# Kernel optimization log

Measured on AMD Instinct MI355X. Metric: run time of the kernel, lower is better.

Reference implementation:

```python
import jax, jax.numpy as jnp
import numpy as np

B, N, C, H, W = 4, 8, 48, 128, 128
DIM = N * C  # 384, must equal in_dim


def conv1x1(x, w, b):
    # x: (B, Cin, H, W), w: (Cout, Cin, 1, 1)
    y = jax.lax.conv_general_dilated(
        x, w, window_strides=(1, 1), padding='VALID',
        dimension_numbers=('NCHW', 'OIHW', 'NCHW'))
    return y + b[None, :, None, None]


def dwconv3x3(x, w, b):
    # depthwise: w: (Cg, 1, 3, 3), groups = Cg
    y = jax.lax.conv_general_dilated(
        x, w, window_strides=(1, 1), padding=((1, 1), (1, 1)),
        dimension_numbers=('NCHW', 'OIHW', 'NCHW'),
        feature_group_count=w.shape[0])
    return y + b[None, :, None, None]


def setup_inputs() -> dict:
    key = jax.random.key(0)
    ks = jax.random.split(key, 4)
    s = 0.02
    return {
        'x': jax.random.normal(ks[0], (B, N, C, H, W), jnp.float32),
        'temperature': jnp.ones((1,), jnp.float32),
        'w_qkv': jax.random.normal(ks[1], (3 * DIM, DIM, 1, 1), jnp.float32) * s,
        'b_qkv': jnp.zeros((3 * DIM,), jnp.float32),
        'w_dw': jax.random.normal(ks[2], (3 * DIM, 1, 3, 3), jnp.float32) * s,
        'b_dw': jnp.zeros((3 * DIM,), jnp.float32),
        'w_proj': jax.random.normal(ks[3], (DIM, DIM, 1, 1), jnp.float32) * s,
        'b_proj': jnp.zeros((DIM,), jnp.float32),
    }


def reference(x, temperature, w_qkv, b_qkv, w_dw, b_dw, w_proj, b_proj):
    b, n, c, h, w = x.shape
    x_in = x.reshape(b, n * c, h, w)
    qkv = dwconv3x3(conv1x1(x_in, w_qkv, b_qkv), w_dw, b_dw)  # (b, 3*n*c, h, w)
    q, k, v = jnp.split(qkv, 3, axis=1)

    def flat(t):
        return t.reshape(b, n, -1)  # (b, n, c*h*w)

    def l2n(t):
        # torch F.normalize: x / max(||x||_2, eps)
        nrm = jnp.sqrt(jnp.sum(t * t, axis=-1, keepdims=True))
        return t / jnp.maximum(nrm, 1e-12)

    q = l2n(flat(q))
    k = l2n(flat(k))
    v = flat(v)
    attn = jax.nn.softmax(jnp.einsum('bnd,bmd->bnm', q, k) * temperature, axis=-1)  # (b, n, n)
    out = jnp.einsum('bnm,bmd->bnd', attn, v).reshape(b, n * c, h, w)
    out = conv1x1(out, w_proj, b_proj)
    out = out.reshape(b, n, c, h, w) + x  # residual
    return out.reshape(b, n * c, h, w)
```

## Files before the change

kernel.cpp:

```cpp
#include <hip/hip_runtime.h>
#include <hip/hip_bf16.h>

#define BB 4
#define CPG 48
#define HH 128
#define WW2 128
#define PP 16384
#define DIM 384
#define DIM3 1152

typedef unsigned short u16;
typedef __attribute__((ext_vector_type(8))) short bf16x8;
typedef __attribute__((ext_vector_type(4))) float f32x4;

__device__ __forceinline__ float bf2f(u16 u) {
    return __uint_as_float(((unsigned int)u) << 16);
}
__device__ __forceinline__ u16 f2bf(float f) {
    unsigned int u = __float_as_uint(f);
    unsigned int r = (u + 0x7fffu + ((u >> 16) & 1u)) >> 16;
    return (u16)r;
}

__device__ __forceinline__ int swz(int row, int kb) {
    return row * 128 + (kb ^ ((row & 7) << 4));
}

__device__ __forceinline__ void gld_lds16(const u16* g, char* l) {
    __builtin_amdgcn_global_load_lds(
        (const __attribute__((address_space(1))) void*)g,
        (__attribute__((address_space(3))) void*)l, 16, 0, 0);
}

__global__ __launch_bounds__(256) void k_wcvt(const float* __restrict__ w,
                                              u16* __restrict__ wbf)
{
    const int i4 = (blockIdx.x * 256 + threadIdx.x) * 4;
    float4 v = *reinterpret_cast<const float4*>(w + i4);
    ushort4 s;
    s.x = f2bf(v.x); s.y = f2bf(v.y); s.z = f2bf(v.z); s.w = f2bf(v.w);
    *reinterpret_cast<ushort4*>(wbf + i4) = s;
}

__global__ __launch_bounds__(256) void k_tr_x(const float* __restrict__ x,
                                              u16* __restrict__ xt)
{
    const int b = blockIdx.z;
    const int k0 = blockIdx.y * 64;
    const int p0 = blockIdx.x * 64;
    const int t = threadIdx.x;
    __shared__ u16 T[64][68];

    const int kl = t >> 4;
    const int pl = (t & 15) * 4;
#pragma unroll
    for (int ks = 0; ks < 4; ++ks) {
        const int k = ks * 16 + kl;
        float4 v = *reinterpret_cast<const float4*>(&x[((size_t)b * DIM + k0 + k) * PP + p0 + pl]);
        ushort4 s;
        s.x = f2bf(v.x); s.y = f2bf(v.y); s.z = f2bf(v.z); s.w = f2bf(v.w);
        *reinterpret_cast<ushort4*>(&T[k][pl]) = s;
    }
    __syncthreads();
    const int pr = t >> 2;
    const int kg = (t & 3) * 16;
    __align__(16) u16 tmp[16];
#pragma unroll
    for (int j = 0; j < 16; ++j) tmp[j] = T[kg + j][pr];
    u16* dst = xt + ((size_t)b * PP + p0 + pr) * DIM + k0 + kg;
    *reinterpret_cast<uint4*>(dst)     = *reinterpret_cast<uint4*>(tmp);
    *reinterpret_cast<uint4*>(dst + 8) = *reinterpret_cast<uint4*>(tmp + 8);
}

template<int MODE>
__global__ __launch_bounds__(256) void k_gemm(const u16* __restrict__ A, int aStride,
                                              const u16* __restrict__ Bt,
                                              const float* __restrict__ bias,
                                              u16* __restrict__ ybf,
                                              const float* __restrict__ xres,
                                              float* __restrict__ fout,
                                              int nyTiles)
{
    const int bid = blockIdx.x;
    const int xcd = bid & 7;
    const int r1  = bid >> 3;
    const int px  = xcd * 16 + (r1 & 15);
    const int r2  = r1 >> 4;
    const int b   = r2 / nyTiles;
    const int yt  = r2 - b * nyTiles;
    const int co0 = yt * 128;
    const int p0  = px * 128;

    const int t   = threadIdx.x;
    const int l   = t & 63;
    const int wid = t >> 6;
    const int wr  = wid >> 1;
    const int wc  = wid & 1;
    const int lr  = l & 15;
    const int lg  = l >> 4;

    __shared__ __align__(16) char lds[32768];
    char* AsB = lds;
    char* BsB = lds + 16384;

    f32x4 acc[4][4];
#pragma unroll
    for (int m = 0; m < 4; ++m)
#pragma unroll
        for (int n = 0; n < 4; ++n) acc[m][n] = (f32x4){0.f, 0.f, 0.f, 0.f};

    const u16* Ab  = A  + (size_t)b * aStride;
    const u16* Btb = Bt + (size_t)b * PP * DIM;

    const int lrow8 = l >> 3;
    const int sl    = l & 7;

    for (int k0 = 0; k0 < DIM; k0 += 64) {
        if (k0) __syncthreads();
#pragma unroll
        for (int i = 0; i < 4; ++i) {
            const int rbase = wid * 32 + i * 8;
            const int row   = rbase + lrow8;
            const int elem  = (sl * 8) ^ ((row & 7) << 3);
            gld_lds16(Ab  + (size_t)(co0 + row) * DIM + k0 + elem, AsB + rbase * 128);
            gld_lds16(Btb + (size_t)(p0  + row) * DIM + k0 + elem, BsB + rbase * 128);
        }
        __syncthreads();

#pragma unroll
        for (int kk = 0; kk < 64; kk += 32) {
            const int kbyte = kk * 2 + lg * 16;
            bf16x8 av[4], bv[4];
#pragma unroll
            for (int m = 0; m < 4; ++m) {
                const int row = wr * 64 + m * 16 + lr;
                av[m] = *reinterpret_cast<const bf16x8*>(AsB + swz(row, kbyte));
            }
#pragma unroll
            for (int n = 0; n < 4; ++n) {
                const int row = wc * 64 + n * 16 + lr;
                bv[n] = *reinterpret_cast<const bf16x8*>(BsB + swz(row, kbyte));
            }
#pragma unroll
            for (int m = 0; m < 4; ++m)
#pragma unroll
                for (int n = 0; n < 4; ++n)
                    acc[m][n] = __builtin_amdgcn_mfma_f32_16x16x32_bf16(
                        av[m], bv[n], acc[m][n], 0, 0, 0);
        }
    }

    float bias_r[4][4];
#pragma unroll
    for (int m = 0; m < 4; ++m)
#pragma unroll
        for (int r = 0; r < 4; ++r)
            bias_r[m][r] = bias[co0 + wr * 64 + m * 16 + lg * 4 + r];

    if (MODE == 0) {
        __syncthreads();
        u16* Cs = reinterpret_cast<u16*>(lds);
#pragma unroll
        for (int m = 0; m < 4; ++m)
#pragma unroll
            for (int n = 0; n < 4; ++n)
#pragma unroll
                for (int r = 0; r < 4; ++r) {
                    const int row = wr * 64 + m * 16 + lg * 4 + r;
                    const int col = wc * 64 + n * 16 + lr;
                    Cs[row * 128 + col] = f2bf(acc[m][n][r] + bias_r[m][r]);
                }
        __syncthreads();
        const int rr = t >> 4;
        const int cs = (t & 15) * 8;
#pragma unroll
        for (int j = 0; j < 8; ++j) {
            const int row = j * 16 + rr;
            *reinterpret_cast<uint4*>(&ybf[((size_t)b * DIM3 + co0 + row) * PP + p0 + cs]) =
                *reinterpret_cast<const uint4*>(&Cs[row * 128 + cs]);
        }
    } else {
        float* Cf = reinterpret_cast<float*>(lds);
#pragma unroll
        for (int h = 0; h < 2; ++h) {
            __syncthreads();
            if (wr == h) {
#pragma unroll
                for (int m = 0; m < 4; ++m)
#pragma unroll
                    for (int n = 0; n < 4; ++n)
#pragma unroll
                        for (int r = 0; r < 4; ++r) {
                            const int lrow = m * 16 + lg * 4 + r;
                            const int col = wc * 64 + n * 16 + lr;
                            Cf[lrow * 128 + col] = acc[m][n][r] + bias_r[m][r];
                        }
            }
            __syncthreads();
            const int rr = t >> 5;
            const int cc = (t & 31) * 4;
#pragma unroll
            for (int j = 0; j < 8; ++j) {
                const int lrow = j * 8 + rr;
                const int grow = h * 64 + lrow;
                const size_t idx = ((size_t)b * DIM + co0 + grow) * PP + p0 + cc;
                float4 xr = *reinterpret_cast<const float4*>(&xres[idx]);
                float4 cv = *reinterpret_cast<const float4*>(&Cf[lrow * 128 + cc]);
                cv.x += xr.x; cv.y += xr.y; cv.z += xr.z; cv.w += xr.w;
                *reinterpret_cast<float4*>(&fout[idx]) = cv;
            }
        }
    }
}

__global__ __launch_bounds__(256) void k_dwtr(const u16* __restrict__ y1,
                                              const float* __restrict__ wdw,
                                              const float* __restrict__ bdw,
                                              u16* __restrict__ vt)
{
    const int b  = blockIdx.z;
    const int cg = blockIdx.y;
    const int p0 = blockIdx.x * 64;
    const int rr = p0 >> 7;
    const int hc = (p0 >> 6) & 1;
    const int t  = (int)threadIdx.x;
    const int ch = t >> 2;
    const int q  = t & 3;
    const int cb = hc * 64 + q * 16;

    const int gch = 2 * DIM + cg * 64 + ch;
    const u16* img = y1 + ((size_t)b * DIM3 + gch) * PP;

    float w9[9];
#pragma unroll
    for (int i = 0; i < 9; ++i) w9[i] = wdw[gch * 9 + i];
    const float bv = bdw[gch];

    __shared__ __align__(16) u16 T[64][72];

    float R[3][18];
#pragma unroll
    for (int dr = 0; dr < 3; ++dr) {
        const int r_ = rr + dr - 1;
        const bool inrow = (r_ >= 0 && r_ < HH);
        if (inrow) {
            union { uint4 v; u16 u[8]; } c0_, c1_;
            c0_.v = *reinterpret_cast<const uint4*>(img + r_ * WW2 + cb);
            c1_.v = *reinterpret_cast<const uint4*>(img + r_ * WW2 + cb + 8);
#pragma unroll
            for (int j = 0; j < 8; ++j) {
                R[dr][1 + j] = bf2f(c0_.u[j]);
                R[dr][9 + j] = bf2f(c1_.u[j]);
            }
        } else {
#pragma unroll
            for (int j = 0; j < 16; ++j) R[dr][1 + j] = 0.f;
        }
        const float lf = __shfl(R[dr][16], t - 1);
        const float rt = __shfl(R[dr][1],  t + 1);
        if (q > 0)           R[dr][0] = lf;
        else if (hc == 1)    R[dr][0] = inrow ? bf2f(img[r_ * WW2 + 63]) : 0.f;
        else                 R[dr][0] = 0.f;
        if (q < 3)           R[dr][17] = rt;
        else if (hc == 0)    R[dr][17] = inrow ? bf2f(img[r_ * WW2 + 64]) : 0.f;
        else                 R[dr][17] = 0.f;
    }

#pragma unroll
    for (int j = 0; j < 16; ++j) {
        float a = bv;
        a = fmaf(w9[0], R[0][j],     a);
        a = fmaf(w9[1], R[0][j + 1], a);
        a = fmaf(w9[2], R[0][j + 2], a);
        a = fmaf(w9[3], R[1][j],     a);
        a = fmaf(w9[4], R[1][j + 1], a);
        a = fmaf(w9[5], R[1][j + 2], a);
        a = fmaf(w9[6], R[2][j],     a);
        a = fmaf(w9[7], R[2][j + 1], a);
        a = fmaf(w9[8], R[2][j + 2], a);
        T[q * 16 + j][ch] = f2bf(a);
    }
    __syncthreads();

    const int pl = t >> 2;
    const int cc = (t & 3) * 16;
    u16* dst = vt + ((size_t)b * PP + p0 + pl) * DIM + cg * 64 + cc;
    *reinterpret_cast<uint4*>(dst)     = *reinterpret_cast<const uint4*>(&T[pl][cc]);
    *reinterpret_cast<uint4*>(dst + 8) = *reinterpret_cast<const uint4*>(&T[pl][cc + 8]);
}

#define LOADROW2(arr, gr_)                                                     \
    {                                                                          \
        const int r_ = (gr_);                                                  \
        if (r_ >= 0 && r_ < HH) {                                              \
            union { uint4 v; u16 u[8]; } cc_;                                  \
            cc_.v = *reinterpret_cast<const uint4*>(img + r_ * WW2 + sp);      \
            arr[1] = bf2f(cc_.u[0]); arr[2] = bf2f(cc_.u[1]);                  \
            arr[3] = bf2f(cc_.u[2]); arr[4] = bf2f(cc_.u[3]);                  \
            arr[5] = bf2f(cc_.u[4]); arr[6] = bf2f(cc_.u[5]);                  \
            arr[7] = bf2f(cc_.u[6]); arr[8] = bf2f(cc_.u[7]);                  \
        } else {                                                               \
            arr[1] = 0.f; arr[2] = 0.f; arr[3] = 0.f; arr[4] = 0.f;            \
            arr[5] = 0.f; arr[6] = 0.f; arr[7] = 0.f; arr[8] = 0.f;            \
        }                                                                      \
        float lf_ = __shfl(arr[8], t - 1);                                     \
        float rt_ = __shfl(arr[1], t + 1);                                     \
        arr[0] = (s > 0)  ? lf_ : 0.f;                                         \
        arr[9] = (s < 15) ? rt_ : 0.f;                                         \
    }

__global__ __launch_bounds__(256) void k_dwqk(const u16* __restrict__ y1,
                                              const float* __restrict__ wdw,
                                              const float* __restrict__ bdw,
                                              float* __restrict__ partial)
{
    const int c    = blockIdx.x;
    const int band = blockIdx.y;
    const int b    = blockIdx.z;
    const int t    = (int)threadIdx.x;
    const int h    = t >> 7;
    const int r    = (t >> 4) & 7;
    const int s    = t & 15;
    const int sp   = s * 8;
    const int r0   = band * 8;

    __shared__ __align__(16) u16 G[16][1032];
    __shared__ __align__(16) float red[4][256];

#pragma unroll
    for (int n = 0; n < 8; ++n) {
        const int gch = h * DIM + n * CPG + c;
        const u16* img = y1 + ((size_t)b * DIM3 + gch) * PP;
        float w9[9];
#pragma unroll
        for (int i = 0; i < 9; ++i) w9[i] = wdw[gch * 9 + i];
        const float bv = bdw[gch];

        float A[10], B[10], C[10];
        LOADROW2(A, r0 + r - 1);
        LOADROW2(B, r0 + r);
        LOADROW2(C, r0 + r + 1);

        union { uint4 v; u16 u[8]; } og;
#pragma unroll
        for (int j = 0; j < 8; ++j) {
            float a = bv;
            a = fmaf(w9[0], A[j],     a);
            a = fmaf(w9[1], A[j + 1], a);
            a = fmaf(w9[2], A[j + 2], a);
            a = fmaf(w9[3], B[j],     a);
            a = fmaf(w9[4], B[j + 1], a);
            a = fmaf(w9[5], B[j + 2], a);
            a = fmaf(w9[6], C[j],     a);
            a = fmaf(w9[7], C[j + 1], a);
            a = fmaf(w9[8], C[j + 2], a);
            og.u[j] = f2bf(a);
        }
        *reinterpret_cast<uint4*>(&G[h * 8 + n][r * 128 + sp]) = og.v;
    }
    __syncthreads();

    const int l = t & 63, w = t >> 6;
    const int grow = l & 15;
    const int koc  = (l >> 4) * 8;
    f32x4 acc = (f32x4){0.f, 0.f, 0.f, 0.f};
#pragma unroll
    for (int q8 = 0; q8 < 8; ++q8) {
        const int koff = w * 256 + q8 * 32 + koc;
        bf16x8 g = *reinterpret_cast<const bf16x8*>(&G[grow][koff]);
        acc = __builtin_amdgcn_mfma_f32_16x16x32_bf16(g, g, acc, 0, 0, 0);
    }
#pragma unroll
    for (int rg = 0; rg < 4; ++rg)
        red[w][((l >> 4) * 4 + rg) * 16 + (l & 15)] = acc[rg];
    __syncthreads();

    const float sum = red[0][t] + red[1][t] + red[2][t] + red[3][t];
    partial[((size_t)((b * 48 + c) * 16 + band)) * 256 + t] = sum;
}

__global__ __launch_bounds__(256) void k_attn(const float* __restrict__ partial,
                                              const float* __restrict__ temp,
                                              float* __restrict__ attn)
{
    const int b = blockIdx.x;
    const int t = threadIdx.x;
    __shared__ float S[256];
    __shared__ float sc[8][8];
    float s = 0.f;
    for (int i = 0; i < 768; ++i)
        s += partial[((size_t)b * 768 + i) * 256 + t];
    S[t] = s;
    __syncthreads();
    if (t < 64) {
        const int n = t >> 3, m = t & 7;
        const float qn = fmaxf(sqrtf(S[n * 16 + n]), 1e-12f);
        const float km = fmaxf(sqrtf(S[(8 + m) * 16 + 8 + m]), 1e-12f);
        sc[n][m] = S[n * 16 + 8 + m] / (qn * km) * temp[0];
    }
    __syncthreads();
    if (t < 8) {
        float mx = -3.0e38f;
#pragma unroll
        for (int m = 0; m < 8; ++m) mx = fmaxf(mx, sc[t][m]);
        float e[8], ssum = 0.f;
#pragma unroll
        for (int m = 0; m < 8; ++m) { e[m] = expf(sc[t][m] - mx); ssum += e[m]; }
        const float inv = 1.f / ssum;
#pragma unroll
        for (int m = 0; m < 8; ++m) attn[(b * 8 + t) * 8 + m] = e[m] * inv;
    }
}

__global__ __launch_bounds__(128) void k_weff(const float* __restrict__ attn,
                                              const float* __restrict__ wproj,
                                              u16* __restrict__ weff)
{
    const int b  = blockIdx.y;
    const int co = blockIdx.x;
    const int t  = threadIdx.x;
    __shared__ float a[64];
    if (t < 64) a[t] = attn[b * 64 + t];
    __syncthreads();
    const float* wrow = wproj + (size_t)co * DIM;
    u16* wout = weff + ((size_t)b * DIM + co) * DIM;
    for (int i = t; i < DIM; i += 128) {
        const int m = i / CPG;
        const int c = i - m * CPG;
        float s = 0.f;
#pragma unroll
        for (int n = 0; n < 8; ++n) s += wrow[n * CPG + c] * a[n * 8 + m];
        wout[i] = f2bf(s);
    }
}

extern "C" void kernel_launch(void* const* d_in, const int* in_sizes, int n_in,
                              void* d_out, int out_size, void* d_ws, size_t ws_size,
                              hipStream_t stream)
{
    const float* x      = (const float*)d_in[0];
    const float* temp   = (const float*)d_in[1];
    const float* w_qkv  = (const float*)d_in[2];
    const float* b_qkv  = (const float*)d_in[3];
    const float* w_dw   = (const float*)d_in[4];
    const float* b_dw   = (const float*)d_in[5];
    const float* w_proj = (const float*)d_in[6];
    const float* b_proj = (const float*)d_in[7];
    float* out = (float*)d_out;

    char* ws = (char*)d_ws;
    const size_t SZ_QKV = (size_t)BB * DIM3 * PP * sizeof(u16);
    const size_t SZ_XT  = (size_t)BB * PP * DIM * sizeof(u16);

    u16* y1 = (u16*)ws;

    u16* xt  = (u16*)(ws + SZ_QKV);
    u16* wbf = (u16*)(ws + SZ_QKV + SZ_XT);
    float* partial = (float*)(ws + SZ_QKV);
    float* attn    = (float*)(ws + SZ_QKV + 3145728);
    u16*   weffb   = (u16*)(ws + SZ_QKV + 3211264);
    u16*   vt      = (u16*)(ws + SZ_QKV + 8388608);

    k_wcvt<<<dim3(DIM3 * DIM / 1024), 256, 0, stream>>>(w_qkv, wbf);
    k_tr_x<<<dim3(PP / 64, DIM / 64, BB), 256, 0, stream>>>(x, xt);
    k_gemm<0><<<dim3(128 * 9 * BB), 256, 0, stream>>>(
        wbf, 0, xt, b_qkv, y1, nullptr, nullptr, 9);
    k_dwtr<<<dim3(PP / 64, DIM / 64, BB), 256, 0, stream>>>(y1, w_dw, b_dw, vt);
    k_dwqk<<<dim3(48, 16, BB), 256, 0, stream>>>(y1, w_dw, b_dw, partial);
    k_attn<<<dim3(BB), 256, 0, stream>>>(partial, temp, attn);
    k_weff<<<dim3(DIM, BB), 128, 0, stream>>>(attn, w_proj, weffb);
    k_gemm<1><<<dim3(128 * 3 * BB), 256, 0, stream>>>(
        weffb, DIM * DIM, vt, b_proj, nullptr, x, out, 3);
}
```

Measured before the change: 286.5 us.

## Restructure depthwise-conv transpose kernel to process 4-row bands with rolling row reuse

After: 266.4 us. -7.0%, faster.

```diff
diff --git a/kernel.cpp b/kernel.cpp
--- a/kernel.cpp
+++ b/kernel.cpp
@@ -213,22 +213,45 @@
     }
 }
 
+#define LOADROW3(arr, gr_)                                                     \
+    {                                                                          \
+        const int r_ = (gr_);                                                  \
+        if (r_ >= 0 && r_ < HH) {                                              \
+            union { uint4 v; u16 u[8]; } a0_, a1_;                             \
+            a0_.v = *reinterpret_cast<const uint4*>(img + r_ * WW2 + c0);      \
+            a1_.v = *reinterpret_cast<const uint4*>(img + r_ * WW2 + c0 + 8);  \
+            arr[1] = bf2f(a0_.u[0]); arr[2] = bf2f(a0_.u[1]);                  \
+            arr[3] = bf2f(a0_.u[2]); arr[4] = bf2f(a0_.u[3]);                  \
+            arr[5] = bf2f(a0_.u[4]); arr[6] = bf2f(a0_.u[5]);                  \
+            arr[7] = bf2f(a0_.u[6]); arr[8] = bf2f(a0_.u[7]);                  \
+            arr[9]  = bf2f(a1_.u[0]); arr[10] = bf2f(a1_.u[1]);                \
+            arr[11] = bf2f(a1_.u[2]); arr[12] = bf2f(a1_.u[3]);                \
+            arr[13] = bf2f(a1_.u[4]); arr[14] = bf2f(a1_.u[5]);                \
+            arr[15] = bf2f(a1_.u[6]); arr[16] = bf2f(a1_.u[7]);                \
+        } else {                                                               \
+            for (int z_ = 1; z_ <= 16; ++z_) arr[z_] = 0.f;                    \
+        }                                                                      \
+        float lf_ = __shfl(arr[16], t - 1);                                    \
+        float rt_ = __shfl(arr[1],  t + 1);                                    \
+        arr[0]  = (s > 0) ? lf_ : 0.f;                                         \
+        arr[17] = (s < 7) ? rt_ : 0.f;                                         \
+    }
+
 __global__ __launch_bounds__(256) void k_dwtr(const u16* __restrict__ y1,
                                               const float* __restrict__ wdw,
                                               const float* __restrict__ bdw,
                                               u16* __restrict__ vt)
 {
-    const int b  = blockIdx.z;
-    const int cg = blockIdx.y;
-    const int p0 = blockIdx.x * 64;
-    const int rr = p0 >> 7;
-    const int hc = (p0 >> 6) & 1;
-    const int t  = (int)threadIdx.x;
-    const int ch = t >> 2;
-    const int q  = t & 3;
-    const int cb = hc * 64 + q * 16;
-
-    const int gch = 2 * DIM + cg * 64 + ch;
+    const int band = blockIdx.x;
+    const int chg  = blockIdx.y;
+    const int b    = blockIdx.z;
+    const int t    = (int)threadIdx.x;
+    const int ch   = t >> 3;
+    const int s    = t & 7;
+    const int c0   = s * 16;
+    const int r0   = band * 4;
+
+    const int gch = 2 * DIM + chg * 32 + ch;
     const u16* img = y1 + ((size_t)b * DIM3 + gch) * PP;
 
     float w9[9];
@@ -236,57 +259,49 @@
     for (int i = 0; i < 9; ++i) w9[i] = wdw[gch * 9 + i];
     const float bv = bdw[gch];
 
-    __shared__ __align__(16) u16 T[64][72];
-
-    float R[3][18];
-#pragma unroll
-    for (int dr = 0; dr < 3; ++dr) {
-        const int r_ = rr + dr - 1;
-        const bool inrow = (r_ >= 0 && r_ < HH);
-        if (inrow) {
-            union { uint4 v; u16 u[8]; } c0_, c1_;
-            c0_.v = *reinterpret_cast<const uint4*>(img + r_ * WW2 + cb);
-            c1_.v = *reinterpret_cast<const uint4*>(img + r_ * WW2 + cb + 8);
-#pragma unroll
-            for (int j = 0; j < 8; ++j) {
-                R[dr][1 + j] = bf2f(c0_.u[j]);
-                R[dr][9 + j] = bf2f(c1_.u[j]);
-            }
-        } else {
-#pragma unroll
-            for (int j = 0; j < 16; ++j) R[dr][1 + j] = 0.f;
-        }
-        const float lf = __shfl(R[dr][16], t - 1);
-        const float rt = __shfl(R[dr][1],  t + 1);
-        if (q > 0)           R[dr][0] = lf;
-        else if (hc == 1)    R[dr][0] = inrow ? bf2f(img[r_ * WW2 + 63]) : 0.f;
-        else                 R[dr][0] = 0.f;
-        if (q < 3)           R[dr][17] = rt;
-        else if (hc == 0)    R[dr][17] = inrow ? bf2f(img[r_ * WW2 + 64]) : 0.f;
-        else                 R[dr][17] = 0.f;
-    }
-
-#pragma unroll
-    for (int j = 0; j < 16; ++j) {
-        float a = bv;
-        a = fmaf(w9[0], R[0][j],     a);
-        a = fmaf(w9[1], R[0][j + 1], a);
-        a = fmaf(w9[2], R[0][j + 2], a);
-        a = fmaf(w9[3], R[1][j],     a);
-        a = fmaf(w9[4], R[1][j + 1], a);
-        a = fmaf(w9[5], R[1][j + 2], a);
-        a = fmaf(w9[6], R[2][j],     a);
-        a = fmaf(w9[7], R[2][j + 1], a);
-        a = fmaf(w9[8], R[2][j + 2], a);
-        T[q * 16 + j][ch] = f2bf(a);
-    }
-    __syncthreads();
-
-    const int pl = t >> 2;
-    const int cc = (t & 3) * 16;
-    u16* dst = vt + ((size_t)b * PP + p0 + pl) * DIM + cg * 64 + cc;
-    *reinterpret_cast<uint4*>(dst)     = *reinterpret_cast<const uint4*>(&T[pl][cc]);
-    *reinterpret_cast<uint4*>(dst + 8) = *reinterpret_cast<const uint4*>(&T[pl][cc + 8]);
+    __shared__ __align__(16) u16 T[32][520];
+
+    float A[18], B[18], C[18];
+    LOADROW3(A, r0 - 1);
+    LOADROW3(B, r0);
+
+#pragma unroll
+    for (int j = 0; j < 4; ++j) {
+        LOADROW3(C, r0 + j + 1);
+        union { uint4 v[2]; u16 u[16]; } og;
+#pragma unroll
+        for (int cidx = 0; cidx < 16; ++cidx) {
+            float a = bv;
+            a = fmaf(w9[0], A[cidx],     a);
+            a = fmaf(w9[1], A[cidx + 1], a);
+            a = fmaf(w9[2], A[cidx + 2], a);
+            a = fmaf(w9[3], B[cidx],     a);
+            a = fmaf(w9[4], B[cidx + 1], a);
+            a = fmaf(w9[5], B[cidx + 2], a);
+            a = fmaf(w9[6], C[cidx],     a);
+            a = fmaf(w9[7], C[cidx + 1], a);
+            a = fmaf(w9[8], C[cidx + 2], a);
+            og.u[cidx] = f2bf(a);
+        }
+        *reinterpret_cast<uint4*>(&T[ch][j * 128 + c0])     = og.v[0];
+        *reinterpret_cast<uint4*>(&T[ch][j * 128 + c0 + 8]) = og.v[1];
+#pragma unroll
+        for (int q = 0; q < 18; ++q) { A[q] = B[q]; B[q] = C[q]; }
+    }
+    __syncthreads();
+
+#pragma unroll
+    for (int j = 0; j < 2; ++j) {
+        const int px = j * 256 + t;
+        union { uint4 v[4]; u16 u[32]; } ov;
+#pragma unroll
+        for (int c2 = 0; c2 < 32; ++c2) ov.u[c2] = T[c2][px];
+        u16* dst = vt + ((size_t)b * PP + band * 512 + px) * DIM + chg * 32;
+        *reinterpret_cast<uint4*>(dst)      = ov.v[0];
+        *reinterpret_cast<uint4*>(dst + 8)  = ov.v[1];
+        *reinterpret_cast<uint4*>(dst + 16) = ov.v[2];
+        *reinterpret_cast<uint4*>(dst + 24) = ov.v[3];
+    }
 }
 
 #define LOADROW2(arr, gr_)                                                     \
@@ -465,7 +480,7 @@
     k_tr_x<<<dim3(PP / 64, DIM / 64, BB), 256, 0, stream>>>(x, xt);
     k_gemm<0><<<dim3(128 * 9 * BB), 256, 0, stream>>>(
         wbf, 0, xt, b_qkv, y1, nullptr, nullptr, 9);
-    k_dwtr<<<dim3(PP / 64, DIM / 64, BB), 256, 0, stream>>>(y1, w_dw, b_dw, vt);
+    k_dwtr<<<dim3(32, 12, BB), 256, 0, stream>>>(y1, w_dw, b_dw, vt);
     k_dwqk<<<dim3(48, 16, BB), 256, 0, stream>>>(y1, w_dw, b_dw, partial);
     k_attn<<<dim3(BB), 256, 0, stream>>>(partial, temp, attn);
     k_weff<<<dim3(DIM, BB), 128, 0, stream>>>(attn, w_proj, weffb);
```
